# Kernel optimization log

Hardware: AMD Instinct MI355X
Metric: run time of the kernel (lower is better)

## Reference

```python
import jax, jax.numpy as jnp
import numpy as np

N, D = 1024, 64  # n_nodes, inputSize == hiddenSize == cellSize


def setup_inputs() -> dict:
    key = jax.random.key(0)
    ks = jax.random.split(key, 9)
    inputs = jax.random.normal(ks[0], (N, D), dtype=jnp.float32)
    # sparse-ish binary adjacency, no self loops
    adj = (jax.random.uniform(ks[1], (N, N)) < 0.03).astype(jnp.float32)
    adj = adj.at[jnp.arange(N), jnp.arange(N)].set(0.0)
    numNei = jnp.maximum(adj.sum(axis=1), 1.0)  # avoid div-by-zero
    # initStates() in torch uses randn for h0/c0
    h0 = jax.random.normal(ks[2], (N, D), dtype=jnp.float32)
    c0 = jax.random.normal(ks[3], (N, D), dtype=jnp.float32)
    # torch nn.Linear default init: U(-1/sqrt(fan_in), 1/sqrt(fan_in))
    s_g = 1.0 / np.sqrt(2 * D)
    s_h = 1.0 / np.sqrt(D)
    Wg = jax.random.uniform(ks[4], (D, 2 * D), minval=-s_g, maxval=s_g, dtype=jnp.float32)
    bg = jax.random.uniform(ks[5], (D,), minval=-s_g, maxval=s_g, dtype=jnp.float32)
    Ws = jax.random.uniform(ks[6], (D, D), minval=-s_h, maxval=s_h, dtype=jnp.float32)
    bs = jax.random.uniform(ks[7], (D,), minval=-s_h, maxval=s_h, dtype=jnp.float32)
    Wn = jax.random.uniform(ks[8], (D, D), minval=-s_h, maxval=s_h, dtype=jnp.float32)
    sequence = jnp.arange(N, dtype=jnp.int32)
    return {"inputs": inputs, "neighbour": adj, "numNei": numNei,
            "h0": h0, "c0": c0, "Wg": Wg, "bg": bg, "Ws": Ws, "bs": bs,
            "Wn": Wn, "sequence": sequence}


def reference(inputs, neighbour, numNei, h0, c0, Wg, bg, Ws, bs, Wn, sequence):
    def step(carry, idx):
        H, C = carry                       # [N, D] each
        inp = inputs[idx]                  # [D]
        h_i = H[idx]                       # [D]
        c_i = C[idx]                       # [D] (torch passes cellState[index])
        nei = neighbour[idx]               # [N] adjacency row
        num = numNei[idx]
        # neighbour-averaged hidden state
        neiH = (nei @ H) / num             # [D]
        pre = jnp.concatenate([inp, h_i]) @ Wg.T + bg + neiH @ Wn.T  # [D]
        inputState = jax.nn.sigmoid(pre)
        outputState = inputState           # identical expression in torch
        helpCell = jnp.tanh(pre)
        fs = inp @ Ws.T + bs               # selfGate(inp), [D]
        # forgetSelfMat broadcast of fs over all nodes
        neiForget = jax.nn.sigmoid(fs[None, :] + H @ Wn.T)   # [N, D]
        forgetState = jax.nn.sigmoid(fs + h_i @ Wn.T)        # [D]
        c_new = (nei @ (neiForget * c_i[None, :])) / num \
                + forgetState * c_i + inputState * helpCell  # [D]
        h_new = jnp.tanh(outputState * c_new)
        return (H.at[idx].set(h_new), C.at[idx].set(c_new)), None

    (Hf, _Cf), _ = jax.lax.scan(step, (h0, c0), sequence)
    # torch: residualHidden aliases hiddenState and is mutated in-place,
    # so `hiddenState + residualHidden` == 2 * final hidden state.
    return Hf + Hf
```

## Files before the change

kernel.cpp:

```cpp
#include <hip/hip_runtime.h>

#define NN 1024
#define DD 64
#define CAP 96
#define SENT 32768
#define NL2E -1.44269504088896f
#define NBLK 8
#define NWAVE (NBLK*16)

typedef __attribute__((ext_vector_type(8))) short bf16x8;
typedef __attribute__((ext_vector_type(4))) float f32x4;

__device__ uint4    WnFragD[8*64];
__device__ float    FSd[NN*DD];
__device__ float    Gd[NN*DD];
__device__ float    preBaseD[NN*DD];
__device__ float    fpreD[NN*DD];
__device__ float4   nodeDatD[NN*DD];
__device__ float    GpubD[(NN+1)*DD];
__device__ int      lowNeiD[NN*CAP + 64];
__device__ int2     hdrD[NN];
__device__ int      posArr[NN];
__device__ float    invNumD[NN];

__device__ __forceinline__ float sigm(float x)  { return 1.0f / (1.0f + __expf(-x)); }
__device__ __forceinline__ float tanhf_(float x){ return 2.0f / (1.0f + __expf(-2.0f*x)) - 1.0f; }
__device__ __forceinline__ unsigned short bf16r(float x) {
  unsigned u = __float_as_uint(x);
  u = u + 0x7fffu + ((u >> 16) & 1u);
  return (unsigned short)(u >> 16);
}

__global__ __launch_bounds__(256) void k_node(const int* __restrict__ seq,
                                              const float* __restrict__ numNei,
                                              const float* __restrict__ inputs,
                                              const float* __restrict__ h0,
                                              const float* __restrict__ Wg,
                                              const float* __restrict__ bg,
                                              const float* __restrict__ Ws,
                                              const float* __restrict__ bs,
                                              const float* __restrict__ Wn) {
  __shared__ float x_l[4][64];
  __shared__ float hh_l[4][64];
  int tid = threadIdx.x;
  int gid = blockIdx.x * 256 + tid;
  if (gid < NN) { posArr[seq[gid]] = gid; invNumD[gid] = 1.0f / numNei[gid]; }
  if (gid < 512) {
    int st = gid >> 6, lane = gid & 63;
    int s = st >> 2, t = st & 3;
    int row = 16*t + (lane & 15);
    int k0 = 32*s + 8*(lane >> 4);
    const float* wr = &Wn[row*64 + k0];
    uint4 f;
    f.x = (unsigned)bf16r(wr[0]) | ((unsigned)bf16r(wr[1]) << 16);
    f.y = (unsigned)bf16r(wr[2]) | ((unsigned)bf16r(wr[3]) << 16);
    f.z = (unsigned)bf16r(wr[4]) | ((unsigned)bf16r(wr[5]) << 16);
    f.w = (unsigned)bf16r(wr[6]) | ((unsigned)bf16r(wr[7]) << 16);
    WnFragD[st*64 + lane] = f;
  }
  if (gid < DD) GpubD[NN*DD + gid] = 0.0f;
  for (int e2 = gid; e2 < NN*CAP; e2 += 256*256) lowNeiD[e2] = SENT;
  int w = tid >> 6, d = tid & 63;
  int i = blockIdx.x * 4 + w;
  x_l[w][d]  = inputs[i*DD + d];
  hh_l[w][d] = h0[i*DD + d];
  __syncthreads();
  float afs = bs[d], apre = bg[d], ag0 = 0.0f;
  const float4* wsr = (const float4*)&Ws[d*64];
  const float4* wnr = (const float4*)&Wn[d*64];
  const float4* wga = (const float4*)&Wg[d*128];
  const float4* wgb = (const float4*)&Wg[d*128 + 64];
  #pragma unroll 4
  for (int k4 = 0; k4 < 16; ++k4) {
    float4 ws4 = wsr[k4], wn4 = wnr[k4], wa4 = wga[k4], wb4 = wgb[k4];
    const float* wsp = (const float*)&ws4;
    const float* wnp = (const float*)&wn4;
    const float* wap = (const float*)&wa4;
    const float* wbp = (const float*)&wb4;
    #pragma unroll
    for (int j = 0; j < 4; ++j) {
      int k = 4*k4 + j;
      float xk = x_l[w][k], hk = hh_l[w][k];
      afs  += xk * wsp[j];
      ag0  += hk * wnp[j];
      apre += xk * wap[j] + hk * wbp[j];
    }
  }
  FSd[i*DD + d]      = afs;
  Gd[i*DD + d]       = ag0;
  preBaseD[i*DD + d] = apre;
  fpreD[i*DD + d]    = sigm(afs + ag0);
}

__global__ __launch_bounds__(256) void k_edges(const float* __restrict__ adj,
                                               const float* __restrict__ c0) {
  int tid = threadIdx.x;
  int w = tid >> 6, d = tid & 63;
  int i = blockIdx.x * 4 + w;
  int pi = posArr[i];
  float fs = FSd[i*DD + d];
  GpubD[i*DD + d] = __int_as_float(0x7FC00000);
  float accP = 0.0f, accS = 0.0f;
  int cnt = 0;
  for (int base = 0; base < NN; base += 64) {
    float a = adj[i*NN + base + d];
    unsigned long long mask = __ballot(a != 0.0f);
    while (mask) {
      int b = __ffsll(mask) - 1;
      mask &= (mask - 1);
      int j = base + b;
      if (posArr[j] < pi) {
        if (d == 0 && cnt < 64) lowNeiD[i*CAP + cnt] = j << 5;
        cnt++;
      } else {
        float g = Gd[j*DD + d];
        accP += g;
        accS += sigm(fs + g);
      }
    }
  }
  float inv = invNumD[i];
  if (d == 0) {
    int ccap = (cnt < 64) ? cnt : 64;
    hdrD[i] = make_int2(ccap, __float_as_int(inv));
  }
  float c0v = c0[i*DD + d];
  float civ = c0v * inv;
  nodeDatD[i*DD + d] = make_float4(NL2E * fs,
                                   preBaseD[i*DD + d] + accP * inv,
                                   civ,
                                   c0v * fpreD[i*DD + d] + civ * accS);
}

__global__ __launch_bounds__(1024, 4) void k_seq(const int* __restrict__ seq,
                                                 float* __restrict__ out) {
  __shared__ unsigned short hstage[16][64];
  int tid  = threadIdx.x;
  int lane = tid & 63, w = tid >> 6;
  int wid  = blockIdx.x * 16 + w;
  uint4 fb[2][4];
  #pragma unroll
  for (int s = 0; s < 2; ++s) {
    #pragma unroll
    for (int t = 0; t < 4; ++t)
      fb[s][t] = WnFragD[(s*4 + t)*64 + lane];
  }

  int p = wid;
  int i = seq[p];
  int2 hd = hdrD[i];
  float4 nd = nodeDatD[i*DD + lane];
  int jbv = lowNeiD[i*CAP + lane];
  int cnt = hd.x;
  float inv = __int_as_float(hd.y);

  #define ALD(c) __hip_atomic_load(&GpubD[((c) << 1) + lane], __ATOMIC_RELAXED, __HIP_MEMORY_SCOPE_AGENT)

  for (;;) {
    int pn = p + NWAVE;
    bool more = (pn < NN);
    int i2 = 0, cnt2 = 0, jbv2 = 0;
    float inv2 = 0.0f;
    float4 nd2 = {0.f, 0.f, 0.f, 0.f};
    if (more) {
      i2 = seq[pn];
      int2 hd2 = hdrD[i2];
      nd2  = nodeDatD[i2*DD + lane];
      jbv2 = lowNeiD[i2*CAP + lane];
      cnt2 = hd2.x;
      inv2 = __int_as_float(hd2.y);
    }
    float fs2n = nd.x;
    float accG, accS;
    do {
      accG = 0.0f; accS = 0.0f;
      float g0[8], g1[8], g2[8], g3[8];
      if (cnt > 0) {
        #pragma unroll
        for (int q = 0; q < 8; ++q) g0[q] = ALD(__builtin_amdgcn_readlane(jbv, q));
      }
      if (cnt > 8) {
        #pragma unroll
        for (int q = 0; q < 8; ++q) g1[q] = ALD(__builtin_amdgcn_readlane(jbv, 8 + q));
      }
      if (cnt > 16) {
        #pragma unroll
        for (int q = 0; q < 8; ++q) g2[q] = ALD(__builtin_amdgcn_readlane(jbv, 16 + q));
      }
      if (cnt > 24) {
        #pragma unroll
        for (int q = 0; q < 8; ++q) g3[q] = ALD(__builtin_amdgcn_readlane(jbv, 24 + q));
      }
      auto domath = [&](float G) {
        float x_ = __builtin_fmaf(G, NL2E, fs2n);
        float e_ = __builtin_amdgcn_exp2f(x_);
        accS += __builtin_amdgcn_rcpf(1.0f + e_);
        accG += G;
      };
      if (cnt > 0) {
        #pragma unroll
        for (int q = 0; q < 8; ++q) domath(g0[q]);
      }
      if (cnt > 8) {
        #pragma unroll
        for (int q = 0; q < 8; ++q) domath(g1[q]);
      }
      if (cnt > 16) {
        #pragma unroll
        for (int q = 0; q < 8; ++q) domath(g2[q]);
      }
      if (cnt > 24) {
        #pragma unroll
        for (int q = 0; q < 8; ++q) domath(g3[q]);
      }
      if (cnt > 32) {
        for (int base = 32; base < cnt; base += 8) {
          float gg[8];
          #pragma unroll
          for (int q = 0; q < 8; ++q) gg[q] = ALD(__builtin_amdgcn_readlane(jbv, base + q));
          #pragma unroll
          for (int q = 0; q < 8; ++q) domath(gg[q]);
        }
      }
    } while (__any((accG != accG) || (accS != accS)));
    {
      int npad = (8 - (cnt & 7)) & 7;
      float sig0 = __builtin_amdgcn_rcpf(1.0f + __builtin_amdgcn_exp2f(fs2n));
      accS -= (float)npad * sig0;
    }
    float pre = nd.y + inv * accG;
    float is  = sigm(pre);
    float hcl = tanhf_(pre);
    float c   = nd.z * accS + nd.w + is * hcl;
    float h   = tanhf_(is * c);
    hstage[w][lane] = bf16r(h);
    const uint4* hv = (const uint4*)&hstage[w][0];
    uint4 fa0 = hv[lane >> 4];
    uint4 fa1 = hv[4 + (lane >> 4)];
    f32x4 z = {0.f, 0.f, 0.f, 0.f};
    f32x4 a0 = __builtin_amdgcn_mfma_f32_16x16x32_bf16(__builtin_bit_cast(bf16x8, fa0), __builtin_bit_cast(bf16x8, fb[0][0]), z, 0, 0, 0);
    f32x4 a1 = __builtin_amdgcn_mfma_f32_16x16x32_bf16(__builtin_bit_cast(bf16x8, fa0), __builtin_bit_cast(bf16x8, fb[0][1]), z, 0, 0, 0);
    f32x4 a2 = __builtin_amdgcn_mfma_f32_16x16x32_bf16(__builtin_bit_cast(bf16x8, fa0), __builtin_bit_cast(bf16x8, fb[0][2]), z, 0, 0, 0);
    f32x4 a3 = __builtin_amdgcn_mfma_f32_16x16x32_bf16(__builtin_bit_cast(bf16x8, fa0), __builtin_bit_cast(bf16x8, fb[0][3]), z, 0, 0, 0);
    a0 = __builtin_amdgcn_mfma_f32_16x16x32_bf16(__builtin_bit_cast(bf16x8, fa1), __builtin_bit_cast(bf16x8, fb[1][0]), a0, 0, 0, 0);
    a1 = __builtin_amdgcn_mfma_f32_16x16x32_bf16(__builtin_bit_cast(bf16x8, fa1), __builtin_bit_cast(bf16x8, fb[1][1]), a1, 0, 0, 0);
    a2 = __builtin_amdgcn_mfma_f32_16x16x32_bf16(__builtin_bit_cast(bf16x8, fa1), __builtin_bit_cast(bf16x8, fb[1][2]), a2, 0, 0, 0);
    a3 = __builtin_amdgcn_mfma_f32_16x16x32_bf16(__builtin_bit_cast(bf16x8, fa1), __builtin_bit_cast(bf16x8, fb[1][3]), a3, 0, 0, 0);
    float r01 = (lane & 16) ? a1[0] : a0[0];
    float r23 = (lane & 16) ? a3[0] : a2[0];
    float rg  = (lane & 32) ? r23 : r01;
    __hip_atomic_store(&GpubD[(i << 6) + lane], rg, __ATOMIC_RELAXED, __HIP_MEMORY_SCOPE_AGENT);
    out[i*DD + lane] = 2.0f * h;
    if (!more) break;
    p = pn; i = i2; cnt = cnt2; inv = inv2; nd = nd2; jbv = jbv2;
  }
  #undef ALD
}

extern "C" void kernel_launch(void* const* d_in, const int* in_sizes, int n_in,
                              void* d_out, int out_size, void* d_ws, size_t ws_size,
                              hipStream_t stream) {
  const float* inputs = (const float*)d_in[0];
  const float* adj    = (const float*)d_in[1];
  const float* numNei = (const float*)d_in[2];
  const float* h0     = (const float*)d_in[3];
  const float* c0     = (const float*)d_in[4];
  const float* Wg     = (const float*)d_in[5];
  const float* bg     = (const float*)d_in[6];
  const float* Ws     = (const float*)d_in[7];
  const float* bs     = (const float*)d_in[8];
  const float* Wn     = (const float*)d_in[9];
  const int*   seq    = (const int*)d_in[10];
  float* out = (float*)d_out;

  k_node <<<256, 256, 0, stream>>>(seq, numNei, inputs, h0, Wg, bg, Ws, bs, Wn);
  k_edges<<<256, 256, 0, stream>>>(adj, c0);
  k_seq  <<<NBLK, 1024, 0, stream>>>(seq, out);
}
```

Before: 201.8 us.

## Run sequential scan in one workgroup with bf16 LDS-resident G and dynamic work queue

Moves the published per-node G vectors (h·Wnᵀ) from global memory with agent-scope atomics into a bf16 array in LDS. The sequential scan now runs in a single 1024-thread workgroup that claims positions from an LDS atomic counter instead of a fixed stride across 8 blocks. The NaN-sentinel spin now targets only the first missing neighbour, and the sigmoid sums are merged four at a time with a single reciprocal. This aims to cut cross-CU global-memory latency on the dependency chain, at the cost of using only one CU and storing G in bf16.

After: 459.9 us. 2.28x slower.

```diff
diff --git a/kernel.cpp b/kernel.cpp
--- a/kernel.cpp
+++ b/kernel.cpp
@@ -5,8 +5,6 @@
 #define CAP 96
 #define SENT 32768
 #define NL2E -1.44269504088896f
-#define NBLK 8
-#define NWAVE (NBLK*16)
 
 typedef __attribute__((ext_vector_type(8))) short bf16x8;
 typedef __attribute__((ext_vector_type(4))) float f32x4;
@@ -17,7 +15,6 @@
 __device__ float    preBaseD[NN*DD];
 __device__ float    fpreD[NN*DD];
 __device__ float4   nodeDatD[NN*DD];
-__device__ float    GpubD[(NN+1)*DD];
 __device__ int      lowNeiD[NN*CAP + 64];
 __device__ int2     hdrD[NN];
 __device__ int      posArr[NN];
@@ -58,7 +55,6 @@
     f.w = (unsigned)bf16r(wr[6]) | ((unsigned)bf16r(wr[7]) << 16);
     WnFragD[st*64 + lane] = f;
   }
-  if (gid < DD) GpubD[NN*DD + gid] = 0.0f;
   for (int e2 = gid; e2 < NN*CAP; e2 += 256*256) lowNeiD[e2] = SENT;
   int w = tid >> 6, d = tid & 63;
   int i = blockIdx.x * 4 + w;
@@ -99,9 +95,9 @@
   int i = blockIdx.x * 4 + w;
   int pi = posArr[i];
   float fs = FSd[i*DD + d];
-  GpubD[i*DD + d] = __int_as_float(0x7FC00000);
   float accP = 0.0f, accS = 0.0f;
   int cnt = 0;
+  int myj = -1;
   for (int base = 0; base < NN; base += 64) {
     float a = adj[i*NN + base + d];
     unsigned long long mask = __ballot(a != 0.0f);
@@ -110,7 +106,7 @@
       mask &= (mask - 1);
       int j = base + b;
       if (posArr[j] < pi) {
-        if (d == 0 && cnt < 64) lowNeiD[i*CAP + cnt] = j << 5;
+        if (cnt == d) myj = j;
         cnt++;
       } else {
         float g = Gd[j*DD + d];
@@ -119,11 +115,10 @@
       }
     }
   }
+  int ccap = (cnt < 64) ? cnt : 64;
+  if (d < ccap) lowNeiD[i*CAP + d] = myj << 5;
   float inv = invNumD[i];
-  if (d == 0) {
-    int ccap = (cnt < 64) ? cnt : 64;
-    hdrD[i] = make_int2(ccap, __float_as_int(inv));
-  }
+  if (d == 0) hdrD[i] = make_int2(ccap, __float_as_int(inv));
   float c0v = c0[i*DD + d];
   float civ = c0v * inv;
   nodeDatD[i*DD + d] = make_float4(NL2E * fs,
@@ -134,10 +129,18 @@
 
 __global__ __launch_bounds__(1024, 4) void k_seq(const int* __restrict__ seq,
                                                  float* __restrict__ out) {
+  __shared__ unsigned long long Gl64[(NN*DD + 64)/4];
+  __shared__ int seqL[NN];
   __shared__ unsigned short hstage[16][64];
+  __shared__ int head;
+  unsigned short* Gl = (unsigned short*)Gl64;
   int tid  = threadIdx.x;
   int lane = tid & 63, w = tid >> 6;
-  int wid  = blockIdx.x * 16 + w;
+  if (tid == 0) head = 0;
+  seqL[tid] = seq[tid];
+  #pragma unroll
+  for (int q = 0; q < 16; ++q) Gl64[q*1024 + tid] = 0x7FC07FC07FC07FC0ull;
+  if (tid < 16) Gl64[NN*DD/4 + tid] = 0ull;
   uint4 fb[2][4];
   #pragma unroll
   for (int s = 0; s < 2; ++s) {
@@ -145,88 +148,142 @@
     for (int t = 0; t < 4; ++t)
       fb[s][t] = WnFragD[(s*4 + t)*64 + lane];
   }
-
-  int p = wid;
-  int i = seq[p];
-  int2 hd = hdrD[i];
-  float4 nd = nodeDatD[i*DD + lane];
-  int jbv = lowNeiD[i*CAP + lane];
-  int cnt = hd.x;
-  float inv = __int_as_float(hd.y);
-
-  #define ALD(c) __hip_atomic_load(&GpubD[((c) << 1) + lane], __ATOMIC_RELAXED, __HIP_MEMORY_SCOPE_AGENT)
+  __syncthreads();
+
+  int    iA, cntA, jbA;
+  float  invA;
+  float4 ndA;
+  #define ISSUE(DST_i, DST_cnt, DST_jb, DST_inv, DST_nd, P) do {      \
+    DST_i   = seqL[P];                                                \
+    int2 hd_ = hdrD[DST_i];                                           \
+    DST_nd  = nodeDatD[DST_i*DD + lane];                              \
+    DST_jb  = lowNeiD[DST_i*CAP + lane];                              \
+    DST_cnt = hd_.x;                                                  \
+    DST_inv = __int_as_float(hd_.y);                                  \
+  } while (0)
+
+  int t0 = 0;
+  if (lane == 0) t0 = __hip_atomic_fetch_add(&head, 1, __ATOMIC_RELAXED, __HIP_MEMORY_SCOPE_WORKGROUP);
+  int p = __builtin_amdgcn_readfirstlane(t0);
+  ISSUE(iA, cntA, jbA, invA, ndA, p);
 
   for (;;) {
-    int pn = p + NWAVE;
+    if (lane == 0) t0 = __hip_atomic_fetch_add(&head, 1, __ATOMIC_RELAXED, __HIP_MEMORY_SCOPE_WORKGROUP);
+    int pn = __builtin_amdgcn_readfirstlane(t0);
     bool more = (pn < NN);
-    int i2 = 0, cnt2 = 0, jbv2 = 0;
-    float inv2 = 0.0f;
-    float4 nd2 = {0.f, 0.f, 0.f, 0.f};
-    if (more) {
-      i2 = seq[pn];
-      int2 hd2 = hdrD[i2];
-      nd2  = nodeDatD[i2*DD + lane];
-      jbv2 = lowNeiD[i2*CAP + lane];
-      cnt2 = hd2.x;
-      inv2 = __int_as_float(hd2.y);
-    }
+    int    iB = 0, cntB = 0, jbB = 0;
+    float  invB = 0.0f;
+    float4 ndB = {0.f, 0.f, 0.f, 0.f};
+    if (more) ISSUE(iB, cntB, jbB, invB, ndB, pn);
+
+    const int   i   = iA;
+    const int   cnt = cntA;
+    const int   jb  = jbA;
+    const float inv = invA;
+    const float4 nd = ndA;
     float fs2n = nd.x;
     float accG, accS;
-    do {
+    float g[32];
+    #define LDN(c)  __uint_as_float(((unsigned)Gl[((c) << 1) + lane]) << 16)
+    #define LDA_(c) __uint_as_float(((unsigned)__hip_atomic_load(&Gl[((c) << 1) + lane], __ATOMIC_RELAXED, __HIP_MEMORY_SCOPE_WORKGROUP)) << 16)
+    #define GFILL(LD_) do {                                                       \
+      if (cnt > 0)  { g[0] =LD_(__builtin_amdgcn_readlane(jb, 0));                \
+                      g[1] =LD_(__builtin_amdgcn_readlane(jb, 1));                \
+                      g[2] =LD_(__builtin_amdgcn_readlane(jb, 2));                \
+                      g[3] =LD_(__builtin_amdgcn_readlane(jb, 3)); }              \
+      if (cnt > 4)  { g[4] =LD_(__builtin_amdgcn_readlane(jb, 4));                \
+                      g[5] =LD_(__builtin_amdgcn_readlane(jb, 5));                \
+                      g[6] =LD_(__builtin_amdgcn_readlane(jb, 6));                \
+                      g[7] =LD_(__builtin_amdgcn_readlane(jb, 7)); }              \
+      if (cnt > 8)  { g[8] =LD_(__builtin_amdgcn_readlane(jb, 8));                \
+                      g[9] =LD_(__builtin_amdgcn_readlane(jb, 9));                \
+                      g[10]=LD_(__builtin_amdgcn_readlane(jb,10));                \
+                      g[11]=LD_(__builtin_amdgcn_readlane(jb,11)); }              \
+      if (cnt > 12) { g[12]=LD_(__builtin_amdgcn_readlane(jb,12));                \
+                      g[13]=LD_(__builtin_amdgcn_readlane(jb,13));                \
+                      g[14]=LD_(__builtin_amdgcn_readlane(jb,14));                \
+                      g[15]=LD_(__builtin_amdgcn_readlane(jb,15)); }              \
+      if (cnt > 16) { g[16]=LD_(__builtin_amdgcn_readlane(jb,16));                \
+                      g[17]=LD_(__builtin_amdgcn_readlane(jb,17));                \
+                      g[18]=LD_(__builtin_amdgcn_readlane(jb,18));                \
+                      g[19]=LD_(__builtin_amdgcn_readlane(jb,19)); }              \
+      if (cnt > 20) { g[20]=LD_(__builtin_amdgcn_readlane(jb,20));                \
+                      g[21]=LD_(__builtin_amdgcn_readlane(jb,21));                \
+                      g[22]=LD_(__builtin_amdgcn_readlane(jb,22));                \
+                      g[23]=LD_(__builtin_amdgcn_readlane(jb,23)); }              \
+      if (cnt > 24) { g[24]=LD_(__builtin_amdgcn_readlane(jb,24));                \
+                      g[25]=LD_(__builtin_amdgcn_readlane(jb,25));                \
+                      g[26]=LD_(__builtin_amdgcn_readlane(jb,26));                \
+                      g[27]=LD_(__builtin_amdgcn_readlane(jb,27)); }              \
+      if (cnt > 28) { g[28]=LD_(__builtin_amdgcn_readlane(jb,28));                \
+                      g[29]=LD_(__builtin_amdgcn_readlane(jb,29));                \
+                      g[30]=LD_(__builtin_amdgcn_readlane(jb,30));                \
+                      g[31]=LD_(__builtin_amdgcn_readlane(jb,31)); }              \
+    } while (0)
+
+    auto quad = [&](float ga, float gb, float gc, float gd) {
+      float xa = fminf(__builtin_fmaf(ga, NL2E, fs2n), 25.0f);
+      float xb = fminf(__builtin_fmaf(gb, NL2E, fs2n), 25.0f);
+      float xc = fminf(__builtin_fmaf(gc, NL2E, fs2n), 25.0f);
+      float xd = fminf(__builtin_fmaf(gd, NL2E, fs2n), 25.0f);
+      float ea = __builtin_amdgcn_exp2f(xa);
+      float eb = __builtin_amdgcn_exp2f(xb);
+      float ec = __builtin_amdgcn_exp2f(xc);
+      float ed = __builtin_amdgcn_exp2f(xd);
+      float s0 = ea + eb, n0 = s0 + 2.0f;
+      float d0 = __builtin_fmaf(ea, eb, s0) + 1.0f;
+      float s1 = ec + ed, n1 = s1 + 2.0f;
+      float d1 = __builtin_fmaf(ec, ed, s1) + 1.0f;
+      float Nn = __builtin_fmaf(n0, d1, n1 * d0);
+      float Dd = d0 * d1;
+      accS = __builtin_fmaf(Nn, __builtin_amdgcn_rcpf(Dd), accS);
+      accG += (ga + gb) + (gc + gd);
+    };
+
+    bool redo = false;
+    for (;;) {
       accG = 0.0f; accS = 0.0f;
-      float g0[8], g1[8], g2[8], g3[8];
-      if (cnt > 0) {
-        #pragma unroll
-        for (int q = 0; q < 8; ++q) g0[q] = ALD(__builtin_amdgcn_readlane(jbv, q));
-      }
-      if (cnt > 8) {
-        #pragma unroll
-        for (int q = 0; q < 8; ++q) g1[q] = ALD(__builtin_amdgcn_readlane(jbv, 8 + q));
-      }
-      if (cnt > 16) {
-        #pragma unroll
-        for (int q = 0; q < 8; ++q) g2[q] = ALD(__builtin_amdgcn_readlane(jbv, 16 + q));
-      }
-      if (cnt > 24) {
-        #pragma unroll
-        for (int q = 0; q < 8; ++q) g3[q] = ALD(__builtin_amdgcn_readlane(jbv, 24 + q));
-      }
-      auto domath = [&](float G) {
-        float x_ = __builtin_fmaf(G, NL2E, fs2n);
-        float e_ = __builtin_amdgcn_exp2f(x_);
-        accS += __builtin_amdgcn_rcpf(1.0f + e_);
-        accG += G;
-      };
-      if (cnt > 0) {
-        #pragma unroll
-        for (int q = 0; q < 8; ++q) domath(g0[q]);
-      }
-      if (cnt > 8) {
-        #pragma unroll
-        for (int q = 0; q < 8; ++q) domath(g1[q]);
-      }
-      if (cnt > 16) {
-        #pragma unroll
-        for (int q = 0; q < 8; ++q) domath(g2[q]);
-      }
-      if (cnt > 24) {
-        #pragma unroll
-        for (int q = 0; q < 8; ++q) domath(g3[q]);
-      }
+      if (!redo) GFILL(LDN); else GFILL(LDA_);
+      if (cnt > 0)  quad(g[0],  g[1],  g[2],  g[3]);
+      if (cnt > 4)  quad(g[4],  g[5],  g[6],  g[7]);
+      if (cnt > 8)  quad(g[8],  g[9],  g[10], g[11]);
+      if (cnt > 12) quad(g[12], g[13], g[14], g[15]);
+      if (cnt > 16) quad(g[16], g[17], g[18], g[19]);
+      if (cnt > 20) quad(g[20], g[21], g[22], g[23]);
+      if (cnt > 24) quad(g[24], g[25], g[26], g[27]);
+      if (cnt > 28) quad(g[28], g[29], g[30], g[31]);
       if (cnt > 32) {
-        for (int base = 32; base < cnt; base += 8) {
-          float gg[8];
-          #pragma unroll
-          for (int q = 0; q < 8; ++q) gg[q] = ALD(__builtin_amdgcn_readlane(jbv, base + q));
-          #pragma unroll
-          for (int q = 0; q < 8; ++q) domath(gg[q]);
+        for (int base = 32; base < cnt; base += 4) {
+          float ga, gb, gc, gd;
+          for (;;) {
+            ga = LDA_(__builtin_amdgcn_readlane(jb, base));
+            gb = LDA_(__builtin_amdgcn_readlane(jb, base + 1));
+            gc = LDA_(__builtin_amdgcn_readlane(jb, base + 2));
+            gd = LDA_(__builtin_amdgcn_readlane(jb, base + 3));
+            float s = ga + gb + gc + gd;
+            if (!__any(s != s)) break;
+          }
+          quad(ga, gb, gc, gd);
         }
       }
-    } while (__any((accG != accG) || (accS != accS)));
+      if (!__any(accG != accG)) break;
+      int qm = 0;
+      #pragma unroll
+      for (int q = 31; q >= 0; --q) {
+        if (q < cnt && __any(g[q] != g[q])) qm = q;
+      }
+      int jm = __builtin_amdgcn_readlane(jb, qm);
+      for (;;) {
+        unsigned short gv = __hip_atomic_load(&Gl[(jm << 1) + lane], __ATOMIC_RELAXED, __HIP_MEMORY_SCOPE_WORKGROUP);
+        if (!__any(gv == (unsigned short)0x7FC0)) break;
+      }
+      redo = true;
+    }
     {
-      int npad = (8 - (cnt & 7)) & 7;
-      float sig0 = __builtin_amdgcn_rcpf(1.0f + __builtin_amdgcn_exp2f(fs2n));
-      accS -= (float)npad * sig0;
+      int slots = (cnt <= 32) ? ((cnt + 3) & ~3) : (32 + ((cnt - 32 + 3) & ~3));
+      float e0   = __builtin_amdgcn_exp2f(fminf(fs2n, 25.0f));
+      float sig0 = __builtin_amdgcn_rcpf(1.0f + e0);
+      accS -= (float)(slots - cnt) * sig0;
     }
     float pre = nd.y + inv * accG;
     float is  = sigm(pre);
@@ -249,12 +306,15 @@
     float r01 = (lane & 16) ? a1[0] : a0[0];
     float r23 = (lane & 16) ? a3[0] : a2[0];
     float rg  = (lane & 32) ? r23 : r01;
-    __hip_atomic_store(&GpubD[(i << 6) + lane], rg, __ATOMIC_RELAXED, __HIP_MEMORY_SCOPE_AGENT);
+    Gl[(i << 6) + lane] = bf16r(rg);
     out[i*DD + lane] = 2.0f * h;
     if (!more) break;
-    p = pn; i = i2; cnt = cnt2; inv = inv2; nd = nd2; jbv = jbv2;
-  }
-  #undef ALD
+    iA = iB; cntA = cntB; jbA = jbB; invA = invB; ndA = ndB;
+    #undef GFILL
+    #undef LDN
+    #undef LDA_
+  }
+  #undef ISSUE
 }
 
 extern "C" void kernel_launch(void* const* d_in, const int* in_sizes, int n_in,
@@ -275,5 +335,5 @@
 
   k_node <<<256, 256, 0, stream>>>(seq, numNei, inputs, h0, Wg, bg, Ws, bs, Wn);
   k_edges<<<256, 256, 0, stream>>>(adj, c0);
-  k_seq  <<<NBLK, 1024, 0, stream>>>(seq, out);
-}
+  k_seq  <<<1, 1024, 0, stream>>>(seq, out);
+}
```
